# Performance work log

Hardware: AMD Instinct MI355X
Metric: run time of the kernel (lower is better)

## Reference

```python
import jax, jax.numpy as jnp
import numpy as np
from jax import lax

L = 32          # lattice side
H = 128         # net_width / hidden_size
B = 512         # batch_size
EPS = 1e-8


def setup_inputs() -> dict:
    key = jax.random.key(0)
    k0, k1, k2, k3, k4 = jax.random.split(key, 5)
    # binary spin configurations in {0., 1.}
    samples = jnp.round(jax.random.uniform(k0, (B, L, L))).astype(jnp.float32)
    s1 = 1.0 / np.sqrt(H + 2)
    # per-cell linear1 weights: input = cat([x(2), h(H)]) -> H
    W1 = jax.random.uniform(k1, (L * L, H, H + 2), minval=-s1, maxval=s1, dtype=jnp.float32)
    b1 = jax.random.uniform(k2, (L * L, H), minval=-s1, maxval=s1, dtype=jnp.float32)
    sf = 1.0 / np.sqrt(H)
    # per-cell fc head: H -> 1
    Wf = jax.random.uniform(k3, (L * L, H), minval=-sf, maxval=sf, dtype=jnp.float32)
    bf = jax.random.uniform(k4, (L * L,), minval=-sf, maxval=sf, dtype=jnp.float32)
    return {"samples": samples, "W1": W1, "b1": b1, "Wf": Wf, "bf": bf}


def _log_prob(samples, W1, b1, Wf, bf):
    Bsz = samples.shape[0]
    dt = samples.dtype
    W1 = W1.reshape(L, L, H, H + 2)
    b1 = b1.reshape(L, L, H)
    Wf = Wf.reshape(L, L, H)
    bf = bf.reshape(L, L)

    rows = jnp.transpose(samples, (1, 0, 2))                       # (L, B, L)
    prev = jnp.concatenate([jnp.zeros((1, Bsz, L), dt), rows[:-1]], axis=0)  # row above (x_v); zeros for row 0
    parity = (jnp.arange(L) % 2) == 1                              # odd rows scan right-to-left (zigzag)

    def row_step(h_v, xs):
        cur, pv, p, Wr, br, wfr, bfr = xs
        # reorder everything into visitation order (reverse for odd rows)
        cur_o = jnp.where(p, cur[:, ::-1], cur)     # (B, L) current-row spins / mask
        pv_o = jnp.where(p, pv[:, ::-1], pv)        # (B, L) spins of row above (x_v)
        hv_o = jnp.where(p, h_v[::-1], h_v)         # (L, B, H) vertical hidden states
        Wr_o = jnp.where(p, Wr[::-1], Wr)
        br_o = jnp.where(p, br[::-1], br)
        wf_o = jnp.where(p, wfr[::-1], wfr)
        bf_o = jnp.where(p, bfr[::-1], bfr)
        # horizontal input x_h = previously visited spin in this row (0 at row start)
        xh = jnp.concatenate([jnp.zeros((Bsz, 1), dt), cur_o[:, :-1]], axis=1)  # (B, L)

        def cell(h_h, cxs):
            xh_j, xv_j, m_j, hv_j, W, b, wf, bfs = cxs
            xh_s = jnp.stack([xh_j, 1.0 - xh_j], axis=1)   # (B, 2)
            xv_s = jnp.stack([xv_j, 1.0 - xv_j], axis=1)   # (B, 2)
            # linear1 applied to both (x_h,h_h) and (x_v,h_v); linear2 is unused in the original forward
            inp = jnp.concatenate([xh_s, h_h], axis=1) + jnp.concatenate([xv_s, hv_j], axis=1)  # (B, H+2)
            h = jnp.tanh(inp @ W.T + 2.0 * b)              # (B, H)
            x_hat = jax.nn.sigmoid(h @ wf + bfs)           # (B,)
            lp = jnp.log(x_hat + EPS) * m_j + jnp.log(1.0 - x_hat + EPS) * (1.0 - m_j)
            return h, (h, lp)

        cxs = (xh.T, pv_o.T, cur_o.T, hv_o, Wr_o, br_o, wf_o, bf_o)
        _, (hs, lps) = lax.scan(cell, jnp.zeros((Bsz, H), dt), cxs)
        h_v_new = jnp.where(p, hs[::-1], hs)               # back to raw column order
        return h_v_new, lps.sum(axis=0)                    # (B,) row log-prob

    h_v0 = jnp.zeros((L, Bsz, H), dt)
    _, row_lps = lax.scan(row_step, h_v0, (rows, prev, parity, W1, b1, Wf, bf))
    return row_lps.sum(axis=0)                             # (B,)


def reference(samples, W1, b1, Wf, bf):
    return _log_prob(samples, W1, b1, Wf, bf)
```

## Files before the change

kernel.cpp:

```cpp
#include <hip/hip_runtime.h>
#include <math.h>
#include <stdint.h>

#define Lr 32
#define Hh 128
#define NCELL (Lr * Lr)
#define NEPS 1e-8f
#define CELLB 33792

typedef _Float16 f16;
typedef f16 h2 __attribute__((ext_vector_type(2)));
typedef uint32_t u32;
typedef u32 u32x4 __attribute__((ext_vector_type(4)));
typedef u32 u32x2 __attribute__((ext_vector_type(2)));

__device__ __forceinline__ void bar_lds() {
    asm volatile("s_waitcnt lgkmcnt(0)\n\ts_barrier" ::: "memory");
}

template<int CTRL>
__device__ __forceinline__ float dpp_get(float x) {
    return __int_as_float(__builtin_amdgcn_update_dpp(
        0, __float_as_int(x), CTRL, 0xf, 0xf, true));
}

__device__ __forceinline__ float rlane(float x, int l) {
    return __int_as_float(__builtin_amdgcn_readlane(__float_as_int(x), l));
}

__device__ __forceinline__ float dot2(h2 a, h2 b, float c) {
    return __builtin_amdgcn_fdot2(a, b, c, false);
}

__device__ __forceinline__ h2 bch2(u32 v) {
    union { u32 u; h2 h; } cv; cv.u = v; return cv.h;
}
__device__ __forceinline__ float h16(u32 w, int hi) {
    union { unsigned short u; f16 h; } c;
    c.u = (unsigned short)(hi ? (w >> 16) : (w & 0xffff));
    return (float)c.h;
}

__device__ __forceinline__ float fast_tanh(float x) {
    x = fminf(9.f, fmaxf(-9.f, x));
    const float e = __expf(2.f * x);
    return 1.f - 2.f / (e + 1.f);
}

__device__ __forceinline__ int cell_of(int s) {
    const int i = s >> 5, jj = s & 31;
    const int c = (i & 1) ? (Lr - 1 - jj) : jj;
    return i * Lr + c;
}

__global__ __launch_bounds__(256)
void transpose_w(const float* __restrict__ W1, const float* __restrict__ b1,
                 const float* __restrict__ Wf, char* __restrict__ Wt) {
    __shared__ float tile[Hh * 130];
    const int cell = blockIdx.x;
    const float* src = W1 + (size_t)cell * (Hh * 130);
    for (int idx = threadIdx.x; idx < Hh * 130; idx += 256)
        tile[idx] = src[idx];
    __syncthreads();
    char* dst = Wt + (size_t)cell * CELLB;
    const int t = threadIdx.x;
    for (int idx = t; idx < 2048; idx += 256) {
        const int c4 = idx >> 9, tt = idx & 511;
        const int kk = tt >> 2, q = tt & 3;
        union { u32x4 v; f16 h[8]; } o;
        for (int j = 0; j < 4; ++j) {
            const int p = q * 16 + c4 * 4 + j;
            o.h[2 * j]     = (f16)tile[kk * 130 + 2 + 2 * p];
            o.h[2 * j + 1] = (f16)tile[kk * 130 + 3 + 2 * p];
        }
        *(u32x4*)(dst + c4 * 8192 + tt * 16) = o.v;
    }
    if (t < Hh) {
        union { u32x2 v; f16 h[4]; } o;
        const float w0 = tile[t * 130 + 0], w1 = tile[t * 130 + 1];
        const float bb = 2.f * b1[cell * Hh + t];
        o.h[0] = (f16)(2.f * w1 + bb);
        o.h[1] = (f16)(w0 + w1 + bb);
        o.h[2] = (f16)(2.f * w0 + bb);
        o.h[3] = (f16)Wf[cell * Hh + t];
        *(u32x2*)(dst + 32768 + t * 8) = o.v;
    }
}

__global__ __launch_bounds__(512, 4)
void rnn2d(const float* __restrict__ samples,
           const char* __restrict__ Wt,
           const float* __restrict__ bfv,
           float* __restrict__ out)
{
    __shared__ __align__(16) h2  inp[2][64];
    __shared__ __align__(16) f16 hvh[Lr * Hh];
    __shared__ float smp[NCELL];
    __shared__ float bfs[NCELL];
    __shared__ __align__(16) float fp_[2][8];
    __shared__ int   sidx[2];
    __shared__ float lpb[2];

    const int t = threadIdx.x;
    const int k = t >> 2;
    const int q = t & 3;
    const int w = t >> 6;
    const int b = blockIdx.x;

    u32 vc[4], vt;
    for (int c4 = 0; c4 < 4; ++c4) vc[c4] = (u32)(c4 * 8192 + t * 16);
    vt = (u32)(32768 + k * 8);

    {
        f16* z1 = (f16*)inp;
        for (int idx = t; idx < 2 * 64 * 2; idx += 512) z1[idx] = (f16)0.f;
        f16* z2 = (f16*)hvh;
        for (int idx = t; idx < Lr * Hh; idx += 512) z2[idx] = (f16)0.f;
        for (int idx = t; idx < NCELL; idx += 512) {
            smp[idx] = samples[(size_t)b * NCELL + idx];
            bfs[idx] = bfv[idx];
        }
        if (t == 0) sidx[0] = 0;
    }
    float lp = 0.f;

    u32x4 A0,A1,A2,A3, B0,B1,B2,B3, C0,C1,C2,C3, D0,D1,D2,D3;
    u32x2 TA, TB, TC, TD;

#define ISSUE(S, W0,W1_,W2_,W3_, TT)                                        \
    {                                                                       \
        const int s_ = ((S) < NCELL) ? (S) : 0;   \
        const char* cb_ = Wt + (size_t)cell_of(s_) * CELLB;                 \
        asm volatile("global_load_dwordx4 %0, %1, %2" : "=v"(W0)  : "v"(vc[0]), "s"(cb_)); \
        asm volatile("global_load_dwordx4 %0, %1, %2" : "=v"(W1_) : "v"(vc[1]), "s"(cb_)); \
        asm volatile("global_load_dwordx4 %0, %1, %2" : "=v"(W2_) : "v"(vc[2]), "s"(cb_)); \
        asm volatile("global_load_dwordx4 %0, %1, %2" : "=v"(W3_) : "v"(vc[3]), "s"(cb_)); \
        asm volatile("global_load_dwordx2 %0, %1, %2" : "=v"(TT)  : "v"(vt),    "s"(cb_)); \
    }

#define WAITP()                                                             \
    asm volatile("s_waitcnt vmcnt(10)" ::: "memory");                       \
    __builtin_amdgcn_sched_barrier(0);

#define DOT4(WQ, QQ, C4)                                                    \
    {                                                                       \
        const u32x4 v_ = (WQ);                                              \
        const uint4 xa_ = *(const uint4*)&inp[QQ][q * 16 + (C4) * 4];       \
        a00 = dot2(bch2(v_.x), bch2(xa_.x), a00);                           \
        a01 = dot2(bch2(v_.y), bch2(xa_.y), a01);                           \
        a02 = dot2(bch2(v_.z), bch2(xa_.z), a02);                           \
        a03 = dot2(bch2(v_.w), bch2(xa_.w), a03);                           \
    }

#define PROC(S, Q, W0,W1_,W2_,W3_, TT)                                      \
    {                                                                       \
        const int i_ = (S) >> 5, j_ = (S) & 31;                             \
        const int c_ = (i_ & 1) ? (Lr - 1 - j_) : j_;                       \
        const int sn_ = ((S) + 1 < NCELL) ? (S) + 1 : (S);                  \
        const int in_ = sn_ >> 5, jn_ = sn_ & 31;                           \
        const int cn_ = (in_ & 1) ? (Lr - 1 - jn_) : jn_;                   \
        const float hvn = (float)hvh[cn_ * Hh + k];                         \
           \
                       \
        if (((t & 63) == 4) && (w == 4 || w == 5) && (S) > 0) {             \
            const int cp_ = cell_of((S) - 1);                               \
            const float4 fa_ = *(const float4*)&fp_[Q][0];                  \
            const float4 fb_ = *(const float4*)&fp_[Q][4];                  \
            const float z_ = ((fa_.x + fa_.y) + (fa_.z + fa_.w))            \
                           + ((fb_.x + fb_.y) + (fb_.z + fb_.w)) + bfs[cp_];\
            const float xh_ = 1.f / (1.f + __expf(-z_));                    \
            const float m_ = smp[cp_];                                      \
            lp += (w == 4) ? __logf(xh_ + NEPS) * m_                        \
                           : __logf(1.f - xh_ + NEPS) * (1.f - m_);         \
        }                                                                   \
           \
        float a00 = 0.f, a01 = 0.f, a02 = 0.f, a03 = 0.f;                   \
        DOT4(W0,  Q, 0) DOT4(W1_, Q, 1)                                     \
        DOT4(W2_, Q, 2) DOT4(W3_, Q, 3)                                     \
        float s0 = (a00 + a01) + (a02 + a03);                               \
        s0 += dpp_get<0xB1>(s0);                    \
        s0 += dpp_get<0x4E>(s0);   \
                     \
        const int sx = sidx[Q];                                             \
        const float t0_ = h16(TT.x, 0), t1_ = h16(TT.x, 1);                 \
        const float t2_ = h16(TT.y, 0), wfv = h16(TT.y, 1);                 \
        s0 += (sx == 2) ? t2_ : ((sx == 1) ? t1_ : t0_);                    \
        const float h0 = fast_tanh(s0);                                     \
            \
           \
        float f0 = h0 * wfv;                                                \
        f0 += dpp_get<0x141>(f0);                                           \
        f0 += dpp_get<0x140>(f0);                                           \
        f0 = f0 + rlane(f0, 16) + rlane(f0, 32) + rlane(f0, 48);            \
        if ((S) + 1 < NCELL) {                                              \
            const float v0 = ((jn_ == 0) ? 0.f : h0)                        \
                           + ((cn_ == c_) ? h0 : hvn);                      \
            const float v0p = __shfl_down(v0, 4);    \
            if ((t & 7) == 0) {                                             \
                h2 u0; u0.x = (f16)v0; u0.y = (f16)v0p;                     \
                inp[(Q) ^ 1][t >> 3] = u0;                                  \
            }                                                               \
            if (t == 0) {                                                   \
                const float xh0 = (jn_ == 0) ? 0.f : smp[i_ * Lr + c_];     \
                const float xv0 = (in_ == 0) ? 0.f                          \
                                             : smp[(in_ - 1) * Lr + cn_];   \
                sidx[(Q) ^ 1] = (int)(xh0 + xv0);                           \
            }                                                               \
        }                                                                   \
        if ((t & 3) == 0) hvh[c_ * Hh + k] = (f16)h0;    \
        if ((t & 63) == 0) fp_[(Q) ^ 1][w] = f0;                            \
        bar_lds();        \
    }

    ISSUE(0, A0,A1,A2,A3, TA);
    ISSUE(1, B0,B1,B2,B3, TB);
    __syncthreads();

    for (int s = 0; s < NCELL; s += 4) {
        ISSUE(s + 2, C0,C1,C2,C3, TC); WAITP();
        PROC(s,     0, A0,A1,A2,A3, TA);
        ISSUE(s + 3, D0,D1,D2,D3, TD); WAITP();
        PROC(s + 1, 1, B0,B1,B2,B3, TB);
        ISSUE(s + 4, A0,A1,A2,A3, TA); WAITP();
        PROC(s + 2, 0, C0,C1,C2,C3, TC);
        ISSUE(s + 5, B0,B1,B2,B3, TB); WAITP();
        PROC(s + 3, 1, D0,D1,D2,D3, TD);
    }
#undef ISSUE
#undef WAITP
#undef DOT4
#undef PROC

    if (((t & 63) == 4) && (w == 4 || w == 5)) {
        const int cp_ = cell_of(NCELL - 1);
        const float4 fa_ = *(const float4*)&fp_[0][0];
        const float4 fb_ = *(const float4*)&fp_[0][4];
        const float z_ = ((fa_.x + fa_.y) + (fa_.z + fa_.w))
                       + ((fb_.x + fb_.y) + (fb_.z + fb_.w)) + bfs[cp_];
        const float xh_ = 1.f / (1.f + __expf(-z_));
        const float m_ = smp[cp_];
        lp += (w == 4) ? __logf(xh_ + NEPS) * m_
                       : __logf(1.f - xh_ + NEPS) * (1.f - m_);
        lpb[w - 4] = lp;
    }
    __syncthreads();
    if (t == 0) out[b] = lpb[0] + lpb[1];
}

extern "C" void kernel_launch(void* const* d_in, const int* in_sizes, int n_in,
                              void* d_out, int out_size, void* d_ws, size_t ws_size,
                              hipStream_t stream) {
    const float* samples = (const float*)d_in[0];
    const float* W1      = (const float*)d_in[1];
    const float* b1      = (const float*)d_in[2];
    const float* Wf      = (const float*)d_in[3];
    const float* bf      = (const float*)d_in[4];
    float* outp = (float*)d_out;
    char* Wt = (char*)d_ws;

    transpose_w<<<1024, 256, 0, stream>>>(W1, b1, Wf, Wt);
    rnn2d<<<512, 512, 0, stream>>>(samples, Wt, bf, outp);
}
```

Before: 1.040 ms.

## Run each batch pair in a single wavefront with LDS-staged weights

Replaces the 512-thread-per-sample recurrence with one 64-lane wavefront that handles two samples. Each lane owns two hidden units and keeps the full input vector in registers. Per-cell weights are streamed into double-buffered LDS with global_load_lds, and the weight layout is repacked so the weights for two hidden units sit together. This removes the block-wide barriers and cross-wave reductions on every sequential step and shares each weight fetch between two samples. In exchange each lane does far more serial dot-product work per step, and only 256 single-wave blocks are launched, which may leave much of the GPU idle.

```diff
diff --git a/kernel.cpp b/kernel.cpp
--- a/kernel.cpp
+++ b/kernel.cpp
@@ -4,7 +4,7 @@
 
 #define Lr 32
 #define Hh 128
-#define NCELL (Lr * Lr)
+#define NCELL 1024
 #define NEPS 1e-8f
 #define CELLB 33792
 
@@ -12,44 +12,40 @@
 typedef f16 h2 __attribute__((ext_vector_type(2)));
 typedef uint32_t u32;
 typedef u32 u32x4 __attribute__((ext_vector_type(4)));
-typedef u32 u32x2 __attribute__((ext_vector_type(2)));
-
-__device__ __forceinline__ void bar_lds() {
-    asm volatile("s_waitcnt lgkmcnt(0)\n\ts_barrier" ::: "memory");
-}
-
+
+#define GLOBAL_AS __attribute__((address_space(1)))
+#define LDS_AS    __attribute__((address_space(3)))
+
+__device__ __forceinline__ h2 bch2(u32 v) {
+    union { u32 u; h2 h; } c; c.u = v; return c.h;
+}
+__device__ __forceinline__ float h16(u32 wd, int hi) {
+    union { unsigned short u; f16 h; } c;
+    c.u = (unsigned short)(hi ? (wd >> 16) : (wd & 0xffff));
+    return (float)c.h;
+}
+__device__ __forceinline__ u32 packh2(float a, float b) {
+    union { u32 u; f16 h[2]; } c; c.h[0] = (f16)a; c.h[1] = (f16)b; return c.u;
+}
+__device__ __forceinline__ float dot2(h2 a, h2 b, float c) {
+    return __builtin_amdgcn_fdot2(a, b, c, false);
+}
 template<int CTRL>
 __device__ __forceinline__ float dpp_get(float x) {
     return __int_as_float(__builtin_amdgcn_update_dpp(
         0, __float_as_int(x), CTRL, 0xf, 0xf, true));
 }
-
 __device__ __forceinline__ float rlane(float x, int l) {
     return __int_as_float(__builtin_amdgcn_readlane(__float_as_int(x), l));
 }
-
-__device__ __forceinline__ float dot2(h2 a, h2 b, float c) {
-    return __builtin_amdgcn_fdot2(a, b, c, false);
-}
-
-__device__ __forceinline__ h2 bch2(u32 v) {
-    union { u32 u; h2 h; } cv; cv.u = v; return cv.h;
-}
-__device__ __forceinline__ float h16(u32 w, int hi) {
-    union { unsigned short u; f16 h; } c;
-    c.u = (unsigned short)(hi ? (w >> 16) : (w & 0xffff));
-    return (float)c.h;
-}
-
 __device__ __forceinline__ float fast_tanh(float x) {
     x = fminf(9.f, fmaxf(-9.f, x));
     const float e = __expf(2.f * x);
     return 1.f - 2.f / (e + 1.f);
 }
-
 __device__ __forceinline__ int cell_of(int s) {
-    const int i = s >> 5, jj = s & 31;
-    const int c = (i & 1) ? (Lr - 1 - jj) : jj;
+    const int i = s >> 5, j = s & 31;
+    const int c = (i & 1) ? (Lr - 1 - j) : j;
     return i * Lr + c;
 }
 
@@ -59,192 +55,193 @@
     __shared__ float tile[Hh * 130];
     const int cell = blockIdx.x;
     const float* src = W1 + (size_t)cell * (Hh * 130);
-    for (int idx = threadIdx.x; idx < Hh * 130; idx += 256)
-        tile[idx] = src[idx];
+    for (int idx = threadIdx.x; idx < Hh * 130; idx += 256) tile[idx] = src[idx];
     __syncthreads();
     char* dst = Wt + (size_t)cell * CELLB;
-    const int t = threadIdx.x;
-    for (int idx = t; idx < 2048; idx += 256) {
-        const int c4 = idx >> 9, tt = idx & 511;
-        const int kk = tt >> 2, q = tt & 3;
+    for (int idx = threadIdx.x; idx < 2048; idx += 256) {
+        const int q = idx >> 6, l = idx & 63;
+        const int k0 = 2 * l, k1 = 2 * l + 1;
+        const int p0 = 2 * q, p1 = 2 * q + 1;
         union { u32x4 v; f16 h[8]; } o;
-        for (int j = 0; j < 4; ++j) {
-            const int p = q * 16 + c4 * 4 + j;
-            o.h[2 * j]     = (f16)tile[kk * 130 + 2 + 2 * p];
-            o.h[2 * j + 1] = (f16)tile[kk * 130 + 3 + 2 * p];
-        }
-        *(u32x4*)(dst + c4 * 8192 + tt * 16) = o.v;
-    }
-    if (t < Hh) {
-        union { u32x2 v; f16 h[4]; } o;
-        const float w0 = tile[t * 130 + 0], w1 = tile[t * 130 + 1];
-        const float bb = 2.f * b1[cell * Hh + t];
-        o.h[0] = (f16)(2.f * w1 + bb);
-        o.h[1] = (f16)(w0 + w1 + bb);
-        o.h[2] = (f16)(2.f * w0 + bb);
-        o.h[3] = (f16)Wf[cell * Hh + t];
-        *(u32x2*)(dst + 32768 + t * 8) = o.v;
-    }
-}
-
-__global__ __launch_bounds__(512, 4)
+        o.h[0] = (f16)tile[k0 * 130 + 2 + 2 * p0];
+        o.h[1] = (f16)tile[k0 * 130 + 3 + 2 * p0];
+        o.h[2] = (f16)tile[k1 * 130 + 2 + 2 * p0];
+        o.h[3] = (f16)tile[k1 * 130 + 3 + 2 * p0];
+        o.h[4] = (f16)tile[k0 * 130 + 2 + 2 * p1];
+        o.h[5] = (f16)tile[k0 * 130 + 3 + 2 * p1];
+        o.h[6] = (f16)tile[k1 * 130 + 2 + 2 * p1];
+        o.h[7] = (f16)tile[k1 * 130 + 3 + 2 * p1];
+        *(u32x4*)(dst + q * 1024 + l * 16) = o.v;
+    }
+    if (threadIdx.x < 64) {
+        const int l = threadIdx.x, k0 = 2 * l, k1 = 2 * l + 1;
+        const float b0 = 2.f * b1[cell * Hh + k0], b1v = 2.f * b1[cell * Hh + k1];
+        union { u32x4 v; f16 h[8]; } o;
+        o.h[0] = (f16)(2.f * tile[k0 * 130 + 1] + b0);
+        o.h[1] = (f16)(2.f * tile[k1 * 130 + 1] + b1v);
+        o.h[2] = (f16)(tile[k0 * 130 + 0] + tile[k0 * 130 + 1] + b0);
+        o.h[3] = (f16)(tile[k1 * 130 + 0] + tile[k1 * 130 + 1] + b1v);
+        o.h[4] = (f16)(2.f * tile[k0 * 130 + 0] + b0);
+        o.h[5] = (f16)(2.f * tile[k1 * 130 + 0] + b1v);
+        o.h[6] = (f16)Wf[cell * Hh + k0];
+        o.h[7] = (f16)Wf[cell * Hh + k1];
+        *(u32x4*)(dst + 32 * 1024 + l * 16) = o.v;
+    }
+}
+
+__global__ __launch_bounds__(64, 1)
 void rnn2d(const float* __restrict__ samples,
            const char* __restrict__ Wt,
            const float* __restrict__ bfv,
            float* __restrict__ out)
 {
-    __shared__ __align__(16) h2  inp[2][64];
-    __shared__ __align__(16) f16 hvh[Lr * Hh];
-    __shared__ float smp[NCELL];
-    __shared__ float bfs[NCELL];
-    __shared__ __align__(16) float fp_[2][8];
-    __shared__ int   sidx[2];
-    __shared__ float lpb[2];
-
-    const int t = threadIdx.x;
-    const int k = t >> 2;
-    const int q = t & 3;
-    const int w = t >> 6;
-    const int b = blockIdx.x;
-
-    u32 vc[4], vt;
-    for (int c4 = 0; c4 < 4; ++c4) vc[c4] = (u32)(c4 * 8192 + t * 16);
-    vt = (u32)(32768 + k * 8);
-
-    {
-        f16* z1 = (f16*)inp;
-        for (int idx = t; idx < 2 * 64 * 2; idx += 512) z1[idx] = (f16)0.f;
-        f16* z2 = (f16*)hvh;
-        for (int idx = t; idx < Lr * Hh; idx += 512) z2[idx] = (f16)0.f;
-        for (int idx = t; idx < NCELL; idx += 512) {
-            smp[idx] = samples[(size_t)b * NCELL + idx];
-            bfs[idx] = bfv[idx];
-        }
-        if (t == 0) sidx[0] = 0;
-    }
-    float lp = 0.f;
-
-    u32x4 A0,A1,A2,A3, B0,B1,B2,B3, C0,C1,C2,C3, D0,D1,D2,D3;
-    u32x2 TA, TB, TC, TD;
-
-#define ISSUE(S, W0,W1_,W2_,W3_, TT)                                        \
+    __shared__ __align__(16) u32 wl[2][8448];
+    __shared__ u32   hvp[2][64 * 33];
+    __shared__ __align__(16) u32 xpb[2][64];
+    __shared__ float smpE[2][NCELL];
+    __shared__ float bfL[NCELL];
+
+    const int t  = threadIdx.x;
+    const int t4 = t * 4;
+    const int b0 = blockIdx.x * 2;
+
+    for (int q = 0; q < 16; ++q) {
+        smpE[0][q * 64 + t] = samples[(size_t)b0 * NCELL + q * 64 + t];
+        smpE[1][q * 64 + t] = samples[(size_t)(b0 + 1) * NCELL + q * 64 + t];
+        bfL[q * 64 + t] = bfv[q * 64 + t];
+    }
+    for (int c = 0; c < 33; ++c) { hvp[0][t * 33 + c] = 0; hvp[1][t * 33 + c] = 0; }
+    xpb[0][t] = 0; xpb[1][t] = 0;
+    asm volatile("s_waitcnt vmcnt(0)" ::: "memory");
+
+    u32x4 xa[16], xc[16];
+#pragma unroll
+    for (int r = 0; r < 16; ++r) { xa[r] = (u32x4)0; xc[r] = (u32x4)0; }
+    float lp0 = 0.f, lp1 = 0.f;
+
+#define STAGE(S, P)                                                         \
     {                                                                       \
-        const int s_ = ((S) < NCELL) ? (S) : 0;   \
+        const int s_ = ((S) < NCELL) ? (S) : 0;                             \
         const char* cb_ = Wt + (size_t)cell_of(s_) * CELLB;                 \
-        asm volatile("global_load_dwordx4 %0, %1, %2" : "=v"(W0)  : "v"(vc[0]), "s"(cb_)); \
-        asm volatile("global_load_dwordx4 %0, %1, %2" : "=v"(W1_) : "v"(vc[1]), "s"(cb_)); \
-        asm volatile("global_load_dwordx4 %0, %1, %2" : "=v"(W2_) : "v"(vc[2]), "s"(cb_)); \
-        asm volatile("global_load_dwordx4 %0, %1, %2" : "=v"(W3_) : "v"(vc[3]), "s"(cb_)); \
-        asm volatile("global_load_dwordx2 %0, %1, %2" : "=v"(TT)  : "v"(vt),    "s"(cb_)); \
-    }
-
-#define WAITP()                                                             \
-    asm volatile("s_waitcnt vmcnt(10)" ::: "memory");                       \
+        _Pragma("unroll")                                                   \
+        for (int q_ = 0; q_ < 33; ++q_)                                     \
+            __builtin_amdgcn_global_load_lds(                               \
+                (const GLOBAL_AS u32*)(cb_ + q_ * 1024 + t * 16),           \
+                (LDS_AS u32*)&wl[P][q_ * 256 + t4], 16, 0, 0);              \
+    }
+
+#define WAITW()                                                             \
+    asm volatile("s_waitcnt vmcnt(33)" ::: "memory");                       \
     __builtin_amdgcn_sched_barrier(0);
 
-#define DOT4(WQ, QQ, C4)                                                    \
+#define PROC(S, Q)                                                          \
     {                                                                       \
-        const u32x4 v_ = (WQ);                                              \
-        const uint4 xa_ = *(const uint4*)&inp[QQ][q * 16 + (C4) * 4];       \
-        a00 = dot2(bch2(v_.x), bch2(xa_.x), a00);                           \
-        a01 = dot2(bch2(v_.y), bch2(xa_.y), a01);                           \
-        a02 = dot2(bch2(v_.z), bch2(xa_.z), a02);                           \
-        a03 = dot2(bch2(v_.w), bch2(xa_.w), a03);                           \
-    }
-
-#define PROC(S, Q, W0,W1_,W2_,W3_, TT)                                      \
-    {                                                                       \
+        STAGE((S) + 1, (Q) ^ 1)                 \
         const int i_ = (S) >> 5, j_ = (S) & 31;                             \
         const int c_ = (i_ & 1) ? (Lr - 1 - j_) : j_;                       \
         const int sn_ = ((S) + 1 < NCELL) ? (S) + 1 : (S);                  \
         const int in_ = sn_ >> 5, jn_ = sn_ & 31;                           \
         const int cn_ = (in_ & 1) ? (Lr - 1 - jn_) : jn_;                   \
-        const float hvn = (float)hvh[cn_ * Hh + k];                         \
-           \
-                       \
-        if (((t & 63) == 4) && (w == 4 || w == 5) && (S) > 0) {             \
-            const int cp_ = cell_of((S) - 1);                               \
-            const float4 fa_ = *(const float4*)&fp_[Q][0];                  \
-            const float4 fb_ = *(const float4*)&fp_[Q][4];                  \
-            const float z_ = ((fa_.x + fa_.y) + (fa_.z + fa_.w))            \
-                           + ((fb_.x + fb_.y) + (fb_.z + fb_.w)) + bfs[cp_];\
-            const float xh_ = 1.f / (1.f + __expf(-z_));                    \
-            const float m_ = smp[cp_];                                      \
-            lp += (w == 4) ? __logf(xh_ + NEPS) * m_                        \
-                           : __logf(1.f - xh_ + NEPS) * (1.f - m_);         \
-        }                                                                   \
-           \
-        float a00 = 0.f, a01 = 0.f, a02 = 0.f, a03 = 0.f;                   \
-        DOT4(W0,  Q, 0) DOT4(W1_, Q, 1)                                     \
-        DOT4(W2_, Q, 2) DOT4(W3_, Q, 3)                                     \
-        float s0 = (a00 + a01) + (a02 + a03);                               \
-        s0 += dpp_get<0xB1>(s0);                    \
-        s0 += dpp_get<0x4E>(s0);   \
-                     \
-        const int sx = sidx[Q];                                             \
-        const float t0_ = h16(TT.x, 0), t1_ = h16(TT.x, 1);                 \
-        const float t2_ = h16(TT.y, 0), wfv = h16(TT.y, 1);                 \
-        s0 += (sx == 2) ? t2_ : ((sx == 1) ? t1_ : t0_);                    \
-        const float h0 = fast_tanh(s0);                                     \
-            \
-           \
-        float f0 = h0 * wfv;                                                \
-        f0 += dpp_get<0x141>(f0);                                           \
-        f0 += dpp_get<0x140>(f0);                                           \
-        f0 = f0 + rlane(f0, 16) + rlane(f0, 32) + rlane(f0, 48);            \
-        if ((S) + 1 < NCELL) {                                              \
-            const float v0 = ((jn_ == 0) ? 0.f : h0)                        \
-                           + ((cn_ == c_) ? h0 : hvn);                      \
-            const float v0p = __shfl_down(v0, 4);    \
-            if ((t & 7) == 0) {                                             \
-                h2 u0; u0.x = (f16)v0; u0.y = (f16)v0p;                     \
-                inp[(Q) ^ 1][t >> 3] = u0;                                  \
-            }                                                               \
-            if (t == 0) {                                                   \
-                const float xh0 = (jn_ == 0) ? 0.f : smp[i_ * Lr + c_];     \
-                const float xv0 = (in_ == 0) ? 0.f                          \
-                                             : smp[(in_ - 1) * Lr + cn_];   \
-                sidx[(Q) ^ 1] = (int)(xh0 + xv0);                           \
+        const int cc_ = i_ * Lr + c_;                                       \
+        const u32 hvn0 = hvp[0][t * 33 + cn_];                              \
+        const u32 hvn1 = hvp[1][t * 33 + cn_];                              \
+        const int il_ = (j_ > 0) ? cell_of((S) - 1) : 0;                    \
+        const float sl0 = (j_ > 0) ? smpE[0][il_] : 0.f;                    \
+        const float sl1 = (j_ > 0) ? smpE[1][il_] : 0.f;                    \
+        const float sa0 = (i_ > 0) ? smpE[0][(i_ - 1) * Lr + c_] : 0.f;     \
+        const float sa1 = (i_ > 0) ? smpE[1][(i_ - 1) * Lr + c_] : 0.f;     \
+        const float bfc = bfL[cc_];                                         \
+        const float m0 = smpE[0][cc_], m1 = smpE[1][cc_];                   \
+        const int cse0 = (int)(sl0 + sa0), cse1 = (int)(sl1 + sa1);         \
+        WAITW()                                                             \
+              \
+        float p0=0.f,p1=0.f,p2=0.f,p3=0.f;     \
+        float r0=0.f,r1=0.f,r2=0.f,r3=0.f;                       \
+        _Pragma("unroll")                                                   \
+        for (int q_ = 0; q_ < 32; ++q_) {                                   \
+            const u32x4 wq = *(const u32x4*)&wl[Q][q_ * 256 + t4];          \
+            const u32x4 ua = xa[q_ >> 1];                                   \
+            const u32x4 uc = xc[q_ >> 1];                                   \
+            const h2 ua0 = bch2(ua[(q_ & 1) * 2]);                          \
+            const h2 ua1 = bch2(ua[(q_ & 1) * 2 + 1]);                      \
+            const h2 uc0 = bch2(uc[(q_ & 1) * 2]);                          \
+            const h2 uc1 = bch2(uc[(q_ & 1) * 2 + 1]);                      \
+            if ((q_ & 1) == 0) {                                            \
+                p0 = dot2(bch2(wq[0]), ua0, p0);                            \
+                p1 = dot2(bch2(wq[1]), ua0, p1);                            \
+                p0 = dot2(bch2(wq[2]), ua1, p0);                            \
+                p1 = dot2(bch2(wq[3]), ua1, p1);                            \
+                r0 = dot2(bch2(wq[0]), uc0, r0);                            \
+                r1 = dot2(bch2(wq[1]), uc0, r1);                            \
+                r0 = dot2(bch2(wq[2]), uc1, r0);                            \
+                r1 = dot2(bch2(wq[3]), uc1, r1);                            \
+            } else {                                                        \
+                p2 = dot2(bch2(wq[0]), ua0, p2);                            \
+                p3 = dot2(bch2(wq[1]), ua0, p3);                            \
+                p2 = dot2(bch2(wq[2]), ua1, p2);                            \
+                p3 = dot2(bch2(wq[3]), ua1, p3);                            \
+                r2 = dot2(bch2(wq[0]), uc0, r2);                            \
+                r3 = dot2(bch2(wq[1]), uc0, r3);                            \
+                r2 = dot2(bch2(wq[2]), uc1, r2);                            \
+                r3 = dot2(bch2(wq[3]), uc1, r3);                            \
             }                                                               \
         }                                                                   \
-        if ((t & 3) == 0) hvh[c_ * Hh + k] = (f16)h0;    \
-        if ((t & 63) == 0) fp_[(Q) ^ 1][w] = f0;                            \
-        bar_lds();        \
-    }
-
-    ISSUE(0, A0,A1,A2,A3, TA);
-    ISSUE(1, B0,B1,B2,B3, TB);
-    __syncthreads();
-
-    for (int s = 0; s < NCELL; s += 4) {
-        ISSUE(s + 2, C0,C1,C2,C3, TC); WAITP();
-        PROC(s,     0, A0,A1,A2,A3, TA);
-        ISSUE(s + 3, D0,D1,D2,D3, TD); WAITP();
-        PROC(s + 1, 1, B0,B1,B2,B3, TB);
-        ISSUE(s + 4, A0,A1,A2,A3, TA); WAITP();
-        PROC(s + 2, 0, C0,C1,C2,C3, TC);
-        ISSUE(s + 5, B0,B1,B2,B3, TB); WAITP();
-        PROC(s + 3, 1, D0,D1,D2,D3, TD);
-    }
-#undef ISSUE
-#undef WAITP
-#undef DOT4
+        const u32x4 tl = *(const u32x4*)&wl[Q][8192 + t4];                  \
+        u32 tt0 = tl[0]; if (cse0 == 1) tt0 = tl[1]; if (cse0 == 2) tt0 = tl[2]; \
+        u32 tt1 = tl[0]; if (cse1 == 1) tt1 = tl[1]; if (cse1 == 2) tt1 = tl[2]; \
+        const float h00 = fast_tanh(p0 + p2 + h16(tt0, 0));                 \
+        const float h01 = fast_tanh(p1 + p3 + h16(tt0, 1));                 \
+        const float h10 = fast_tanh(r0 + r2 + h16(tt1, 0));                 \
+        const float h11 = fast_tanh(r1 + r3 + h16(tt1, 1));                 \
+           \
+        if ((S) + 1 < NCELL) {                                              \
+            const float v00 = ((jn_ == 0) ? 0.f : h00)                      \
+                            + ((cn_ == c_) ? h00 : h16(hvn0, 0));           \
+            const float v01 = ((jn_ == 0) ? 0.f : h01)                      \
+                            + ((cn_ == c_) ? h01 : h16(hvn0, 1));           \
+            const float v10 = ((jn_ == 0) ? 0.f : h10)                      \
+                            + ((cn_ == c_) ? h10 : h16(hvn1, 0));           \
+            const float v11 = ((jn_ == 0) ? 0.f : h11)                      \
+                            + ((cn_ == c_) ? h11 : h16(hvn1, 1));           \
+            xpb[0][t] = packh2(v00, v01);                                   \
+            xpb[1][t] = packh2(v10, v11);                                   \
+            _Pragma("unroll")                                               \
+            for (int r_ = 0; r_ < 16; ++r_) {                               \
+                xa[r_] = *(const u32x4*)&xpb[0][r_ * 4];                    \
+                xc[r_] = *(const u32x4*)&xpb[1][r_ * 4];                    \
+            }                                                               \
+        }                                                                   \
+        hvp[0][t * 33 + c_] = packh2(h00, h01);                             \
+        hvp[1][t * 33 + c_] = packh2(h10, h11);                             \
+         \
+        const float wf0 = h16(tl[3], 0), wf1 = h16(tl[3], 1);               \
+        float f0 = fmaf(h00, wf0, h01 * wf1);                               \
+        float f1 = fmaf(h10, wf0, h11 * wf1);                               \
+        f0 += dpp_get<0xB1>(f0);  f1 += dpp_get<0xB1>(f1);                  \
+        f0 += dpp_get<0x4E>(f0);  f1 += dpp_get<0x4E>(f1);                  \
+        f0 += dpp_get<0x141>(f0); f1 += dpp_get<0x141>(f1);                 \
+        f0 += dpp_get<0x140>(f0); f1 += dpp_get<0x140>(f1);                 \
+        f0 = f0 + rlane(f0, 16) + rlane(f0, 32) + rlane(f0, 48);            \
+        f1 = f1 + rlane(f1, 16) + rlane(f1, 32) + rlane(f1, 48);            \
+        const float xh0 = 1.f / (1.f + __expf(-(f0 + bfc)));                \
+        const float xh1 = 1.f / (1.f + __expf(-(f1 + bfc)));                \
+        lp0 += __logf((m0 > 0.5f) ? (xh0 + NEPS) : (1.f - xh0 + NEPS));     \
+        lp1 += __logf((m1 > 0.5f) ? (xh1 + NEPS) : (1.f - xh1 + NEPS));     \
+    }
+
+    STAGE(0, 0)
+    for (int s = 0; s < NCELL; s += 2) {
+        PROC(s, 0);
+        PROC(s + 1, 1);
+    }
+#undef STAGE
+#undef WAITW
 #undef PROC
 
-    if (((t & 63) == 4) && (w == 4 || w == 5)) {
-        const int cp_ = cell_of(NCELL - 1);
-        const float4 fa_ = *(const float4*)&fp_[0][0];
-        const float4 fb_ = *(const float4*)&fp_[0][4];
-        const float z_ = ((fa_.x + fa_.y) + (fa_.z + fa_.w))
-                       + ((fb_.x + fb_.y) + (fb_.z + fb_.w)) + bfs[cp_];
-        const float xh_ = 1.f / (1.f + __expf(-z_));
-        const float m_ = smp[cp_];
-        lp += (w == 4) ? __logf(xh_ + NEPS) * m_
-                       : __logf(1.f - xh_ + NEPS) * (1.f - m_);
-        lpb[w - 4] = lp;
-    }
-    __syncthreads();
-    if (t == 0) out[b] = lpb[0] + lpb[1];
+    if (t == 0) {
+        out[b0]     = lp0;
+        out[b0 + 1] = lp1;
+    }
 }
 
 extern "C" void kernel_launch(void* const* d_in, const int* in_sizes, int n_in,
@@ -259,5 +256,5 @@
     char* Wt = (char*)d_ws;
 
     transpose_w<<<1024, 256, 0, stream>>>(W1, b1, Wf, Wt);
-    rnn2d<<<512, 512, 0, stream>>>(samples, Wt, bf, outp);
-}
+    rnn2d<<<256, 64, 0, stream>>>(samples, Wt, bf, outp);
+}
```

Result: slower. 2.204 ms (+111.9%).
